# Optimization experiments

Hardware: AMD Instinct MI355X
Metric: run time of the kernel (lower is better)

Reference implementation:

```python
import jax, jax.numpy as jnp
import numpy as np

B, SQ, SK, D, H = 4, 2048, 2048, 1024, 16
HD = D // H
SCALE = HD ** -0.5


def setup_inputs() -> dict:
    key = jax.random.key(0)
    ks = jax.random.split(key, 11)
    s = 0.02
    return {
        "query": jax.random.normal(ks[0], (B, SQ, D), jnp.float32),
        "key": jax.random.normal(ks[1], (B, SK, D), jnp.float32),
        "value": jax.random.normal(ks[2], (B, SK, D), jnp.float32),
        "Wq": jax.random.normal(ks[3], (D, D), jnp.float32) * s,
        "bq": jnp.zeros((D,), jnp.float32),
        "Wk": jax.random.normal(ks[4], (D, D), jnp.float32) * s,
        "bk": jnp.zeros((D,), jnp.float32),
        "Wv": jax.random.normal(ks[5], (D, D), jnp.float32) * s,
        "bv": jnp.zeros((D,), jnp.float32),
        "Wo": jax.random.normal(ks[6], (D, D), jnp.float32) * s,
        "bo": jnp.zeros((D,), jnp.float32),
    }


def reference(query, key, value, Wq, bq, Wk, bk, Wv, bv, Wo, bo):
    # Linear projections (torch nn.Linear: x @ W.T + b)
    Q = query @ Wq.T + bq          # (B, SQ, D)
    K = key @ Wk.T + bk            # (B, SK, D)
    V = value @ Wv.T + bv          # (B, SK, D)
    # split heads -> (B, H, S, HD)
    Q = Q.reshape(B, SQ, H, HD).transpose(0, 2, 1, 3)
    K = K.reshape(B, SK, H, HD).transpose(0, 2, 1, 3)
    V = V.reshape(B, SK, H, HD).transpose(0, 2, 1, 3)
    scores = jnp.einsum('bhqd,bhkd->bhqk', Q, K) * SCALE
    attn = jax.nn.softmax(scores, axis=-1)     # (B, H, SQ, SK); dropout=0 (eval)
    attended = jnp.einsum('bhqk,bhkd->bhqd', attn, V)
    attended = attended.mean(axis=1)           # head-average -> (B, SQ, HD)
    attended = jnp.tile(attended, (1, 1, H))   # repeat to (B, SQ, D)
    output = attended @ Wo.T + bo
    avg_attention = attn.mean(axis=1)          # (B, SQ, SK)
    return (output, avg_attention)
```

## Files before the change

### kernel.cpp

```cpp
#include <hip/hip_runtime.h>
#include <hip/hip_bf16.h>
#include <math.h>

#define BB 4
#define SQL 2048
#define SKL 2048
#define DM 1024
#define NH 16
#define HDIM 64
#define QSCALE 0.18033688011112042f

typedef __attribute__((ext_vector_type(8))) short bf16x8;
typedef __attribute__((ext_vector_type(4))) float f32x4;
typedef __attribute__((ext_vector_type(16))) float f32x16;

__device__ __forceinline__ float exp2fast(float x) { return __builtin_amdgcn_exp2f(x); }
__device__ __forceinline__ float log2fast(float x) { return __builtin_amdgcn_logf(x); }

__device__ __forceinline__ unsigned short f2bf(float f) {
    union { __hip_bfloat16 h; unsigned short u; } c;
    c.h = __float2bfloat16(f);
    return c.u;
}

__device__ __forceinline__ unsigned cvtpk(float lo, float hi) {
    unsigned r;
    asm("v_cvt_pk_bf16_f32 %0, %1, %2" : "=v"(r) : "v"(lo), "v"(hi));
    return r;
}

__device__ __forceinline__ bf16x8 cvt8(const float4& a, const float4& b) {
    bf16x8 r;
    r[0] = (short)f2bf(a.x); r[1] = (short)f2bf(a.y);
    r[2] = (short)f2bf(a.z); r[3] = (short)f2bf(a.w);
    r[4] = (short)f2bf(b.x); r[5] = (short)f2bf(b.y);
    r[6] = (short)f2bf(b.z); r[7] = (short)f2bf(b.w);
    return r;
}

__device__ __forceinline__ void gload16(const void* g, void* l) {
    __builtin_amdgcn_global_load_lds(
        (const __attribute__((address_space(1))) unsigned int*)g,
        (__attribute__((address_space(3))) unsigned int*)l, 16, 0, 0);
}

#define VMCNT0() asm volatile("s_waitcnt vmcnt(0)" ::: "memory")

__global__ __launch_bounds__(256)
void wo_eff_kernel(const float* __restrict__ Wo, float* __restrict__ We) {
    int i = blockIdx.x * 256 + threadIdx.x;
    if (i < DM * HDIM) {
        int n = i >> 6, d = i & 63;
        float s = 0.f;
#pragma unroll
        for (int h = 0; h < NH; ++h) s += Wo[(size_t)n * DM + h * HDIM + d];
        We[i] = s;
    }
}

__global__ __launch_bounds__(256)
void proj_bf16(const float* __restrict__ X, const float* __restrict__ W,
               const float* __restrict__ bias, unsigned short* __restrict__ Y,
               float scale)
{
    __shared__ __align__(16) unsigned short As[128 * 32];
    __shared__ __align__(16) unsigned short Bs[128 * 32];
    const int tid = threadIdx.x;
    const int lane = tid & 63, wid = tid >> 6;
    const int g = lane >> 4, lm = lane & 15;
    const int wr = wid >> 1, wc = wid & 1;
    const int m0 = blockIdx.x * 128, n0 = blockIdx.y * 128;

    int rA[2], cA[2], offA[2];
#pragma unroll
    for (int i = 0; i < 2; ++i) {
        int q = tid + i * 256;
        rA[i] = q >> 2; cA[i] = q & 3;
        offA[i] = rA[i] * 32 + ((cA[i] ^ (rA[i] & 3)) << 3);
    }
    float4 xa[2][2], wa[2][2], xb[2][2], wb[2][2];
#pragma unroll
    for (int i = 0; i < 2; ++i) {
        const float* xp = &X[(size_t)(m0 + rA[i]) * DM + cA[i] * 8];
        const float* wp = &W[(size_t)(n0 + rA[i]) * DM + cA[i] * 8];
        xa[i][0] = *(const float4*)xp; xa[i][1] = *(const float4*)(xp + 4);
        wa[i][0] = *(const float4*)wp; wa[i][1] = *(const float4*)(wp + 4);
    }
    const f32x4 fz = {0.f, 0.f, 0.f, 0.f};
    f32x4 acc[4][4];
#pragma unroll
    for (int i = 0; i < 4; ++i)
#pragma unroll
        for (int j = 0; j < 4; ++j) acc[i][j] = fz;

    for (int t = 0; t < 32; ++t) {
        __syncthreads();
#pragma unroll
        for (int i = 0; i < 2; ++i) {
            *(bf16x8*)&As[offA[i]] = cvt8(xa[i][0], xa[i][1]);
            *(bf16x8*)&Bs[offA[i]] = cvt8(wa[i][0], wa[i][1]);
        }
        if (t < 31) {
            int k0 = (t + 1) * 32;
#pragma unroll
            for (int i = 0; i < 2; ++i) {
                const float* xp = &X[(size_t)(m0 + rA[i]) * DM + k0 + cA[i] * 8];
                const float* wp = &W[(size_t)(n0 + rA[i]) * DM + k0 + cA[i] * 8];
                xb[i][0] = *(const float4*)xp; xb[i][1] = *(const float4*)(xp + 4);
                wb[i][0] = *(const float4*)wp; wb[i][1] = *(const float4*)(wp + 4);
            }
        }
        __syncthreads();
        bf16x8 a[4], b[4];
#pragma unroll
        for (int f = 0; f < 4; ++f) {
            int ra = wr * 64 + f * 16 + lm;
            a[f] = *(const bf16x8*)&As[ra * 32 + (((g) ^ (ra & 3)) << 3)];
            int rb = wc * 64 + f * 16 + lm;
            b[f] = *(const bf16x8*)&Bs[rb * 32 + (((g) ^ (rb & 3)) << 3)];
        }
#pragma unroll
        for (int fm = 0; fm < 4; ++fm)
#pragma unroll
            for (int fn = 0; fn < 4; ++fn)
                acc[fm][fn] = __builtin_amdgcn_mfma_f32_16x16x32_bf16(
                    a[fm], b[fn], acc[fm][fn], 0, 0, 0);
        if (t < 31) {
#pragma unroll
            for (int i = 0; i < 2; ++i) {
                xa[i][0] = xb[i][0]; xa[i][1] = xb[i][1];
                wa[i][0] = wb[i][0]; wa[i][1] = wb[i][1];
            }
        }
    }
    float bn[4];
#pragma unroll
    for (int fn = 0; fn < 4; ++fn) bn[fn] = bias[n0 + wc * 64 + fn * 16 + lm];
#pragma unroll
    for (int fm = 0; fm < 4; ++fm)
#pragma unroll
        for (int i = 0; i < 4; ++i) {
            int m = m0 + wr * 64 + fm * 16 + 4 * g + i;
#pragma unroll
            for (int fn = 0; fn < 4; ++fn) {
                int n = n0 + wc * 64 + fn * 16 + lm;
                Y[(size_t)m * DM + n] = f2bf((acc[fm][fn][i] + bn[fn]) * scale);
            }
        }
}

__global__ __launch_bounds__(256)
void transpose_v(const unsigned short* __restrict__ V, unsigned short* __restrict__ Vt)
{
    __shared__ __align__(16) unsigned short Ts[64][80];
    const int tid = threadIdx.x;
    const int kv0 = blockIdx.x * 64, h = blockIdx.y, b = blockIdx.z;
#pragma unroll
    for (int i = 0; i < 2; ++i) {
        int q = tid + i * 256;
        int r = q >> 3, c = q & 7;
        *(uint4*)&Ts[r][c * 8] =
            *(const uint4*)&V[(size_t)(b * SKL + kv0 + r) * DM + h * HDIM + c * 8];
    }
    __syncthreads();
#pragma unroll
    for (int i = 0; i < 2; ++i) {
        int q = tid + i * 256;
        int d = q >> 3, kc = q & 7;
        union { unsigned short u16[8]; uint4 v; } tw;
#pragma unroll
        for (int e = 0; e < 8; ++e) tw.u16[e] = Ts[kc * 8 + e][d];
        *(uint4*)&Vt[((size_t)(b * NH + h) * HDIM + d) * SKL + kv0 + kc * 8] = tw.v;
    }
}

__global__ __launch_bounds__(256, 2)
void flash_mfma2(const unsigned short* __restrict__ Q,
                 const unsigned short* __restrict__ K,
                 const unsigned short* __restrict__ Vt,
                 float* __restrict__ uw, float* __restrict__ O)
{
    __shared__ __align__(16) unsigned short sK[2][64 * 64];
    __shared__ __align__(16) unsigned short sV[2][64 * 64];
    const int tid = threadIdx.x;
    const int lane = tid & 63, wid = tid >> 6;
    const int l31 = lane & 31, h8 = lane >> 5;
    const int L = blockIdx.x + (blockIdx.y << 3) + (blockIdx.z << 7);
    const int f = ((L & 7) << 6) + (L >> 3);
    const int q0 = (f & 7) * 256;
    const int h = (f >> 3) & 15;
    const int b = f >> 7;
    const int myq0 = q0 + wid * 32 + l31;
    const int myq1 = myq0 + 128;

    bf16x8 qf0[4], qf1[4];
    {
        const unsigned short* qp0 = &Q[(size_t)(b * SQL + myq0) * DM + h * HDIM + h8 * 8];
        const unsigned short* qp1 = &Q[(size_t)(b * SQL + myq1) * DM + h * HDIM + h8 * 8];
#pragma unroll
        for (int c = 0; c < 4; ++c) {
            qf0[c] = *(const bf16x8*)(qp0 + c * 16);
            qf1[c] = *(const bf16x8*)(qp1 + c * 16);
        }
    }

    int rr[2], cc[2];
#pragma unroll
    for (int i = 0; i < 2; ++i) {
        int s = tid + i * 256;
        rr[i] = s >> 3;
        cc[i] = ((s & 7) ^ (rr[i] & 7)) * 8;
    }
    const unsigned short* Kbase = &K[((size_t)b * SKL) * DM + h * HDIM];
    const unsigned short* Vbase = &Vt[((size_t)(b * NH + h) * HDIM) * SKL];

#pragma unroll
    for (int i = 0; i < 2; ++i) {
        gload16(Kbase + (size_t)rr[i] * DM + cc[i], &sK[0][(wid * 64 + i * 256) * 8]);
        gload16(Vbase + (size_t)rr[i] * SKL + cc[i], &sV[0][(wid * 64 + i * 256) * 8]);
    }
    VMCNT0();
    __syncthreads();

    const f32x16 z16 = {0.f};
    f32x16 o00 = z16, o01 = z16, o10 = z16, o11 = z16;
    float l0 = 0.f, l1 = 0.f;
    int cur = 0;

    for (int kt = 0; kt < SKL / 64; ++kt) {
        if (kt + 1 < SKL / 64) {
            int k0 = (kt + 1) * 64;
#pragma unroll
            for (int i = 0; i < 2; ++i) {
                gload16(Kbase + (size_t)(k0 + rr[i]) * DM + cc[i],
                        &sK[cur ^ 1][(wid * 64 + i * 256) * 8]);
                gload16(Vbase + (size_t)rr[i] * SKL + k0 + cc[i],
                        &sV[cur ^ 1][(wid * 64 + i * 256) * 8]);
            }
        }
        f32x16 c00 = z16, c01 = z16, c10 = z16, c11 = z16;
        __builtin_amdgcn_s_setprio(1);
#pragma unroll
        for (int c = 0; c < 4; ++c) {
            int cg = 2 * c + h8;
            bf16x8 a0 = *(const bf16x8*)&sK[cur][l31 * 64 + ((cg ^ (l31 & 7)) << 3)];
            bf16x8 a1 = *(const bf16x8*)&sK[cur][(32 + l31) * 64 + ((cg ^ (l31 & 7)) << 3)];
            c00 = __builtin_amdgcn_mfma_f32_32x32x16_bf16(a0, qf0[c], c00, 0, 0, 0);
            c01 = __builtin_amdgcn_mfma_f32_32x32x16_bf16(a1, qf0[c], c01, 0, 0, 0);
            c10 = __builtin_amdgcn_mfma_f32_32x32x16_bf16(a0, qf1[c], c10, 0, 0, 0);
            c11 = __builtin_amdgcn_mfma_f32_32x32x16_bf16(a1, qf1[c], c11, 0, 0, 0);
        }
        __builtin_amdgcn_s_setprio(0);
        bf16x8 ap0[4], ap1[4];
        {
            float ps = 0.f;
#pragma unroll
            for (int r = 0; r < 16; ++r) { c00[r] = exp2fast(c00[r]); ps += c00[r]; }
#pragma unroll
            for (int r = 0; r < 16; ++r) { c01[r] = exp2fast(c01[r]); ps += c01[r]; }
            l0 += ps;
#pragma unroll
            for (int ks = 0; ks < 4; ++ks) {
                const int base = (ks & 1) * 8;
                const f32x16& ct = (ks & 2) ? c01 : c00;
                unsigned wA0 = cvtpk(ct[base + 0], ct[base + 1]);
                unsigned wA1 = cvtpk(ct[base + 2], ct[base + 3]);
                unsigned wB0 = cvtpk(ct[base + 4], ct[base + 5]);
                unsigned wB1 = cvtpk(ct[base + 6], ct[base + 7]);
                asm volatile("v_permlane32_swap_b32 %0, %1" : "+v"(wA0), "+v"(wB0));
                asm volatile("v_permlane32_swap_b32 %0, %1" : "+v"(wA1), "+v"(wB1));
                union { unsigned u[4]; bf16x8 v; } pu;
                pu.u[0] = wA0; pu.u[1] = wA1; pu.u[2] = wB0; pu.u[3] = wB1;
                ap0[ks] = pu.v;
            }
        }
        {
            float ps = 0.f;
#pragma unroll
            for (int r = 0; r < 16; ++r) { c10[r] = exp2fast(c10[r]); ps += c10[r]; }
#pragma unroll
            for (int r = 0; r < 16; ++r) { c11[r] = exp2fast(c11[r]); ps += c11[r]; }
            l1 += ps;
#pragma unroll
            for (int ks = 0; ks < 4; ++ks) {
                const int base = (ks & 1) * 8;
                const f32x16& ct = (ks & 2) ? c11 : c10;
                unsigned wA0 = cvtpk(ct[base + 0], ct[base + 1]);
                unsigned wA1 = cvtpk(ct[base + 2], ct[base + 3]);
                unsigned wB0 = cvtpk(ct[base + 4], ct[base + 5]);
                unsigned wB1 = cvtpk(ct[base + 6], ct[base + 7]);
                asm volatile("v_permlane32_swap_b32 %0, %1" : "+v"(wA0), "+v"(wB0));
                asm volatile("v_permlane32_swap_b32 %0, %1" : "+v"(wA1), "+v"(wB1));
                union { unsigned u[4]; bf16x8 v; } pu;
                pu.u[0] = wA0; pu.u[1] = wA1; pu.u[2] = wB0; pu.u[3] = wB1;
                ap1[ks] = pu.v;
            }
        }
        __builtin_amdgcn_s_setprio(1);
#pragma unroll
        for (int ks = 0; ks < 4; ++ks) {
            int cg = 2 * ks + h8;
            bf16x8 v0 = *(const bf16x8*)&sV[cur][l31 * 64 + ((cg ^ (l31 & 7)) << 3)];
            bf16x8 v1 = *(const bf16x8*)&sV[cur][(32 + l31) * 64 + ((cg ^ (l31 & 7)) << 3)];
            o00 = __builtin_amdgcn_mfma_f32_32x32x16_bf16(v0, ap0[ks], o00, 0, 0, 0);
            o01 = __builtin_amdgcn_mfma_f32_32x32x16_bf16(v1, ap0[ks], o01, 0, 0, 0);
            o10 = __builtin_amdgcn_mfma_f32_32x32x16_bf16(v0, ap1[ks], o10, 0, 0, 0);
            o11 = __builtin_amdgcn_mfma_f32_32x32x16_bf16(v1, ap1[ks], o11, 0, 0, 0);
        }
        __builtin_amdgcn_s_setprio(0);
        VMCNT0();
        __syncthreads();
        cur ^= 1;
    }

    l0 += __shfl_xor(l0, 32);
    l1 += __shfl_xor(l1, 32);
    if (h8 == 0) {
        uw[(size_t)(b * NH + h) * SQL + myq0] = log2fast(l0 * (float)NH);
        uw[(size_t)(b * NH + h) * SQL + myq1] = log2fast(l1 * (float)NH);
    }
    const float inv0 = 1.0f / (l0 * (float)NH);
    const float inv1 = 1.0f / (l1 * (float)NH);
    float* Op0 = &O[((size_t)(b * NH + h) * SQL + myq0) * HDIM];
    float* Op1 = &O[((size_t)(b * NH + h) * SQL + myq1) * HDIM];
#pragma unroll
    for (int i2 = 0; i2 < 4; ++i2) {
        float4 w0, w1;
        int d = 8 * i2 + 4 * h8;
        w0.x = o00[4 * i2 + 0] * inv0; w0.y = o00[4 * i2 + 1] * inv0;
        w0.z = o00[4 * i2 + 2] * inv0; w0.w = o00[4 * i2 + 3] * inv0;
        w1.x = o01[4 * i2 + 0] * inv0; w1.y = o01[4 * i2 + 1] * inv0;
        w1.z = o01[4 * i2 + 2] * inv0; w1.w = o01[4 * i2 + 3] * inv0;
        *(float4*)(Op0 + d) = w0;
        *(float4*)(Op0 + d + 32) = w1;
        w0.x = o10[4 * i2 + 0] * inv1; w0.y = o10[4 * i2 + 1] * inv1;
        w0.z = o10[4 * i2 + 2] * inv1; w0.w = o10[4 * i2 + 3] * inv1;
        w1.x = o11[4 * i2 + 0] * inv1; w1.y = o11[4 * i2 + 1] * inv1;
        w1.z = o11[4 * i2 + 2] * inv1; w1.w = o11[4 * i2 + 3] * inv1;
        *(float4*)(Op1 + d) = w0;
        *(float4*)(Op1 + d + 32) = w1;
    }
}

__global__ __launch_bounds__(256)
void am_reduce(const float* __restrict__ O, float* __restrict__ am)
{
    int i = blockIdx.x * 256 + threadIdx.x;
    int bq = i >> 4, c = i & 15;
    int b = bq >> 11, q = bq & 2047;
    const float* base = O + ((size_t)b * NH * SQL + q) * HDIM + c * 4;
    float4 s = {0.f, 0.f, 0.f, 0.f};
    for (int h = 0; h < NH; ++h) {
        float4 v = *(const float4*)(base + (size_t)h * SQL * HDIM);
        s.x += v.x; s.y += v.y; s.z += v.z; s.w += v.w;
    }
    *(float4*)(am + (size_t)bq * HDIM + c * 4) = s;
}

__global__ __launch_bounds__(512)
void avg_mfma2(const unsigned short* __restrict__ Q, const unsigned short* __restrict__ K,
               const float* __restrict__ uw, float* __restrict__ avg)
{
    __shared__ __align__(16) unsigned short sQ[2][128 * 64];
    __shared__ __align__(16) unsigned short sK[2][128 * 64];
    __shared__ float uS[NH][128];
    const int tid = threadIdx.x;
    const int lane = tid & 63, wid = tid >> 6;
    const int g = lane >> 4, lm = lane & 15;
    const int wq = wid >> 1, wk = wid & 1;
    const int L = blockIdx.x + (blockIdx.y << 4) + (blockIdx.z << 8);
    const int f = ((L & 7) << 7) + (L >> 3);
    const int k0 = (f & 15) * 128;
    const int q0 = ((f >> 4) & 15) * 128;
    const int b = f >> 8;

    for (int i = tid; i < NH * 128; i += 512) {
        int hh = i >> 7, qq = i & 127;
        uS[hh][qq] = uw[(size_t)(b * NH + hh) * SQL + q0 + qq];
    }

    int rs[2], cs[2];
#pragma unroll
    for (int i = 0; i < 2; ++i) {
        int s = tid + i * 512;
        rs[i] = s >> 3;
        cs[i] = (s & 7) ^ (rs[i] & 7);
    }
    const unsigned short* Qbase = &Q[(size_t)(b * SQL + q0) * DM];
    const unsigned short* Kbase = &K[(size_t)(b * SKL + k0) * DM];
#pragma unroll
    for (int i = 0; i < 2; ++i) {
        gload16(Qbase + (size_t)rs[i] * DM + cs[i] * 8, &sQ[0][(tid + i * 512) * 8]);
        gload16(Kbase + (size_t)rs[i] * DM + cs[i] * 8, &sK[0][(tid + i * 512) * 8]);
    }
    VMCNT0();
    __syncthreads();

    const f32x4 fz = {0.f, 0.f, 0.f, 0.f};
    f32x4 acc[2][4];
#pragma unroll
    for (int mf = 0; mf < 2; ++mf)
#pragma unroll
        for (int nf = 0; nf < 4; ++nf) acc[mf][nf] = fz;

    int cur = 0;
    for (int hh = 0; hh < NH; ++hh) {
        if (hh + 1 < NH) {
#pragma unroll
            for (int i = 0; i < 2; ++i) {
                gload16(Qbase + (size_t)rs[i] * DM + (hh + 1) * HDIM + cs[i] * 8,
                        &sQ[cur ^ 1][(tid + i * 512) * 8]);
                gload16(Kbase + (size_t)rs[i] * DM + (hh + 1) * HDIM + cs[i] * 8,
                        &sK[cur ^ 1][(tid + i * 512) * 8]);
            }
        }
        f32x4 s[2][4];
#pragma unroll
        for (int mf = 0; mf < 2; ++mf)
#pragma unroll
            for (int nf = 0; nf < 4; ++nf) s[mf][nf] = fz;
        __builtin_amdgcn_s_setprio(1);
#pragma unroll
        for (int kk = 0; kk < 2; ++kk) {
            bf16x8 a[2];
#pragma unroll
            for (int mf = 0; mf < 2; ++mf) {
                int ra = wq * 32 + mf * 16 + lm;
                a[mf] = *(const bf16x8*)&sQ[cur][ra * 64 + (((kk * 4 + g) ^ (ra & 7)) << 3)];
            }
#pragma unroll
            for (int nf = 0; nf < 4; ++nf) {
                int rb = wk * 64 + nf * 16 + lm;
                bf16x8 kb = *(const bf16x8*)&sK[cur][rb * 64 + (((kk * 4 + g) ^ (rb & 7)) << 3)];
#pragma unroll
                for (int mf = 0; mf < 2; ++mf)
                    s[mf][nf] = __builtin_amdgcn_mfma_f32_16x16x32_bf16(
                        a[mf], kb, s[mf][nf], 0, 0, 0);
            }
        }
        __builtin_amdgcn_s_setprio(0);
#pragma unroll
        for (int mf = 0; mf < 2; ++mf)
#pragma unroll
            for (int i4 = 0; i4 < 4; ++i4) {
                float u = uS[hh][wq * 32 + mf * 16 + 4 * g + i4];
#pragma unroll
                for (int nf = 0; nf < 4; ++nf)
                    acc[mf][nf][i4] += exp2fast(s[mf][nf][i4] - u);
            }
        VMCNT0();
        __syncthreads();
        cur ^= 1;
    }
#pragma unroll
    for (int mf = 0; mf < 2; ++mf)
#pragma unroll
        for (int i4 = 0; i4 < 4; ++i4) {
            int qrow = q0 + wq * 32 + mf * 16 + 4 * g + i4;
#pragma unroll
            for (int nf = 0; nf < 4; ++nf)
                avg[(size_t)(b * SQL + qrow) * SKL + k0 + wk * 64 + nf * 16 + lm] =
                    acc[mf][nf][i4];
        }
}

__global__ __launch_bounds__(256)
void out_gemm(const float* __restrict__ amp, const float* __restrict__ We,
              const float* __restrict__ bo, float* __restrict__ out)
{
    __shared__ float As[64][68];
    __shared__ float Bs[64][68];
    const int m0 = blockIdx.x << 6, n0 = blockIdx.y << 6;
    const int tid = threadIdx.x;
    const int tx = tid & 15, ty = tid >> 4;
    const int lrow = tid >> 4, ldc = (tid & 15) << 2;
#pragma unroll
    for (int rr = 0; rr < 4; ++rr) {
        int r = (rr << 4) + lrow;
        float4 a = *reinterpret_cast<const float4*>(&amp[(size_t)(m0 + r) * HDIM + ldc]);
        float4 w = *reinterpret_cast<const float4*>(&We[(size_t)(n0 + r) * HDIM + ldc]);
        As[ldc + 0][r] = a.x; As[ldc + 1][r] = a.y; As[ldc + 2][r] = a.z; As[ldc + 3][r] = a.w;
        Bs[ldc + 0][r] = w.x; Bs[ldc + 1][r] = w.y; Bs[ldc + 2][r] = w.z; Bs[ldc + 3][r] = w.w;
    }
    __syncthreads();
    float acc[4][4] = {};
    for (int d = 0; d < 64; ++d) {
        float4 av = *reinterpret_cast<const float4*>(&As[d][ty << 2]);
        float4 bv = *reinterpret_cast<const float4*>(&Bs[d][tx << 2]);
        float aa[4] = {av.x, av.y, av.z, av.w};
        float bb[4] = {bv.x, bv.y, bv.z, bv.w};
#pragma unroll
        for (int i = 0; i < 4; ++i)
#pragma unroll
            for (int j = 0; j < 4; ++j)
                acc[i][j] = fmaf(aa[i], bb[j], acc[i][j]);
    }
    float4 bv = *reinterpret_cast<const float4*>(&bo[n0 + (tx << 2)]);
    float bb4[4] = {bv.x, bv.y, bv.z, bv.w};
#pragma unroll
    for (int i = 0; i < 4; ++i) {
        int m = m0 + (ty << 2) + i;
        float4 o = make_float4(acc[i][0] + bb4[0], acc[i][1] + bb4[1],
                               acc[i][2] + bb4[2], acc[i][3] + bb4[3]);
        *reinterpret_cast<float4*>(&out[(size_t)m * DM + n0 + (tx << 2)]) = o;
    }
}

extern "C" void kernel_launch(void* const* d_in, const int* in_sizes, int n_in,
                              void* d_out, int out_size, void* d_ws, size_t ws_size,
                              hipStream_t stream)
{
    const float* query = (const float*)d_in[0];
    const float* key   = (const float*)d_in[1];
    const float* value = (const float*)d_in[2];
    const float* Wq = (const float*)d_in[3];
    const float* bq = (const float*)d_in[4];
    const float* Wk = (const float*)d_in[5];
    const float* bk = (const float*)d_in[6];
    const float* Wv = (const float*)d_in[7];
    const float* bv = (const float*)d_in[8];
    const float* Wo = (const float*)d_in[9];
    const float* bo = (const float*)d_in[10];

    float* out0 = (float*)d_out;
    float* out_avg = out0 + (size_t)BB * SQL * DM;

    const size_t nQ = (size_t)BB * SQL * DM;
    const size_t nML = (size_t)BB * NH * SQL;
    const size_t nAM = (size_t)BB * SQL * HDIM;
    unsigned short* Qb = (unsigned short*)d_ws;
    unsigned short* Kb = Qb + nQ;
    unsigned short* Vb = Kb + nQ;
    unsigned short* Vt = Vb + nQ;
    float* Ob  = (float*)(Vt + nQ);
    float* uw  = Ob + (size_t)BB * NH * SQL * HDIM;
    float* amb = uw + nML;
    float* We  = amb + nAM;

    dim3 blk(256);
    wo_eff_kernel<<<dim3((DM * HDIM + 255) / 256), blk, 0, stream>>>(Wo, We);

    dim3 gp(64, 8);
    proj_bf16<<<gp, blk, 0, stream>>>(query, Wq, bq, Qb, QSCALE);
    proj_bf16<<<gp, blk, 0, stream>>>(key,   Wk, bk, Kb, 1.0f);
    proj_bf16<<<gp, blk, 0, stream>>>(value, Wv, bv, Vb, 1.0f);

    transpose_v<<<dim3(32, 16, 4), blk, 0, stream>>>(Vb, Vt);
    flash_mfma2<<<dim3(SQL / 256, NH, BB), blk, 0, stream>>>(Qb, Kb, Vt, uw, Ob);
    am_reduce<<<dim3(512), blk, 0, stream>>>(Ob, amb);
    avg_mfma2<<<dim3(SKL / 128, SQL / 128, BB), dim3(512), 0, stream>>>(Qb, Kb, uw, out_avg);
    out_gemm<<<dim3(128, 16), blk, 0, stream>>>(amb, We, bo, out0);
}
```

Baseline: 297.0 us.

## Use 128-key tiles in flash kernel and interleave PV with softmax; relayout O

```diff
diff --git a/kernel.cpp b/kernel.cpp
--- a/kernel.cpp
+++ b/kernel.cpp
@@ -180,8 +180,8 @@
                  const unsigned short* __restrict__ Vt,
                  float* __restrict__ uw, float* __restrict__ O)
 {
-    __shared__ __align__(16) unsigned short sK[2][64 * 64];
-    __shared__ __align__(16) unsigned short sV[2][64 * 64];
+    __shared__ __align__(16) unsigned short sK[2][128 * 64];
+    __shared__ __align__(16) unsigned short sV[2][64 * 128];
     const int tid = threadIdx.x;
     const int lane = tid & 63, wid = tid >> 6;
     const int l31 = lane & 31, h8 = lane >> 5;
@@ -204,20 +204,22 @@
         }
     }
 
-    int rr[2], cc[2];
-#pragma unroll
-    for (int i = 0; i < 2; ++i) {
+    int krr[4], kcc[4], vrr[4], vcc[4];
+#pragma unroll
+    for (int i = 0; i < 4; ++i) {
         int s = tid + i * 256;
-        rr[i] = s >> 3;
-        cc[i] = ((s & 7) ^ (rr[i] & 7)) * 8;
+        krr[i] = s >> 3;
+        kcc[i] = ((s & 7) ^ (krr[i] & 7)) * 8;
+        vrr[i] = s >> 4;
+        vcc[i] = ((s & 15) ^ (vrr[i] & 15)) * 8;
     }
     const unsigned short* Kbase = &K[((size_t)b * SKL) * DM + h * HDIM];
     const unsigned short* Vbase = &Vt[((size_t)(b * NH + h) * HDIM) * SKL];
 
 #pragma unroll
-    for (int i = 0; i < 2; ++i) {
-        gload16(Kbase + (size_t)rr[i] * DM + cc[i], &sK[0][(wid * 64 + i * 256) * 8]);
-        gload16(Vbase + (size_t)rr[i] * SKL + cc[i], &sV[0][(wid * 64 + i * 256) * 8]);
+    for (int i = 0; i < 4; ++i) {
+        gload16(Kbase + (size_t)krr[i] * DM + kcc[i], &sK[0][(wid * 64 + i * 256) * 8]);
+        gload16(Vbase + (size_t)vrr[i] * SKL + vcc[i], &sV[0][(wid * 64 + i * 256) * 8]);
     }
     VMCNT0();
     __syncthreads();
@@ -227,87 +229,99 @@
     float l0 = 0.f, l1 = 0.f;
     int cur = 0;
 
-    for (int kt = 0; kt < SKL / 64; ++kt) {
-        if (kt + 1 < SKL / 64) {
-            int k0 = (kt + 1) * 64;
-#pragma unroll
-            for (int i = 0; i < 2; ++i) {
-                gload16(Kbase + (size_t)(k0 + rr[i]) * DM + cc[i],
+    for (int kt = 0; kt < SKL / 128; ++kt) {
+        if (kt + 1 < SKL / 128) {
+            int kk0 = (kt + 1) * 128;
+#pragma unroll
+            for (int i = 0; i < 4; ++i) {
+                gload16(Kbase + (size_t)(kk0 + krr[i]) * DM + kcc[i],
                         &sK[cur ^ 1][(wid * 64 + i * 256) * 8]);
-                gload16(Vbase + (size_t)rr[i] * SKL + k0 + cc[i],
+                gload16(Vbase + (size_t)vrr[i] * SKL + kk0 + vcc[i],
                         &sV[cur ^ 1][(wid * 64 + i * 256) * 8]);
             }
         }
-        f32x16 c00 = z16, c01 = z16, c10 = z16, c11 = z16;
-        __builtin_amdgcn_s_setprio(1);
-#pragma unroll
-        for (int c = 0; c < 4; ++c) {
-            int cg = 2 * c + h8;
-            bf16x8 a0 = *(const bf16x8*)&sK[cur][l31 * 64 + ((cg ^ (l31 & 7)) << 3)];
-            bf16x8 a1 = *(const bf16x8*)&sK[cur][(32 + l31) * 64 + ((cg ^ (l31 & 7)) << 3)];
-            c00 = __builtin_amdgcn_mfma_f32_32x32x16_bf16(a0, qf0[c], c00, 0, 0, 0);
-            c01 = __builtin_amdgcn_mfma_f32_32x32x16_bf16(a1, qf0[c], c01, 0, 0, 0);
-            c10 = __builtin_amdgcn_mfma_f32_32x32x16_bf16(a0, qf1[c], c10, 0, 0, 0);
-            c11 = __builtin_amdgcn_mfma_f32_32x32x16_bf16(a1, qf1[c], c11, 0, 0, 0);
-        }
-        __builtin_amdgcn_s_setprio(0);
-        bf16x8 ap0[4], ap1[4];
         {
+            f32x16 c[4] = {z16, z16, z16, z16};
+            __builtin_amdgcn_s_setprio(1);
+#pragma unroll
+            for (int dc = 0; dc < 4; ++dc) {
+                int cg = 2 * dc + h8;
+#pragma unroll
+                for (int j = 0; j < 4; ++j) {
+                    int r = 32 * j + l31;
+                    bf16x8 a = *(const bf16x8*)&sK[cur][r * 64 + ((cg ^ (r & 7)) << 3)];
+                    c[j] = __builtin_amdgcn_mfma_f32_32x32x16_bf16(a, qf0[dc], c[j], 0, 0, 0);
+                }
+            }
+            __builtin_amdgcn_s_setprio(0);
             float ps = 0.f;
 #pragma unroll
-            for (int r = 0; r < 16; ++r) { c00[r] = exp2fast(c00[r]); ps += c00[r]; }
-#pragma unroll
-            for (int r = 0; r < 16; ++r) { c01[r] = exp2fast(c01[r]); ps += c01[r]; }
+            for (int j = 0; j < 4; ++j)
+#pragma unroll
+                for (int r = 0; r < 16; ++r) { c[j][r] = exp2fast(c[j][r]); ps += c[j][r]; }
             l0 += ps;
-#pragma unroll
-            for (int ks = 0; ks < 4; ++ks) {
-                const int base = (ks & 1) * 8;
-                const f32x16& ct = (ks & 2) ? c01 : c00;
-                unsigned wA0 = cvtpk(ct[base + 0], ct[base + 1]);
-                unsigned wA1 = cvtpk(ct[base + 2], ct[base + 3]);
-                unsigned wB0 = cvtpk(ct[base + 4], ct[base + 5]);
-                unsigned wB1 = cvtpk(ct[base + 6], ct[base + 7]);
+            __builtin_amdgcn_s_setprio(1);
+#pragma unroll
+            for (int ks = 0; ks < 8; ++ks) {
+                const int j = ks >> 1, base = (ks & 1) * 8;
+                unsigned wA0 = cvtpk(c[j][base + 0], c[j][base + 1]);
+                unsigned wA1 = cvtpk(c[j][base + 2], c[j][base + 3]);
+                unsigned wB0 = cvtpk(c[j][base + 4], c[j][base + 5]);
+                unsigned wB1 = cvtpk(c[j][base + 6], c[j][base + 7]);
                 asm volatile("v_permlane32_swap_b32 %0, %1" : "+v"(wA0), "+v"(wB0));
                 asm volatile("v_permlane32_swap_b32 %0, %1" : "+v"(wA1), "+v"(wB1));
                 union { unsigned u[4]; bf16x8 v; } pu;
                 pu.u[0] = wA0; pu.u[1] = wA1; pu.u[2] = wB0; pu.u[3] = wB1;
-                ap0[ks] = pu.v;
-            }
+                int ch = 2 * ks + h8;
+                int r0 = l31, r1 = 32 + l31;
+                bf16x8 v0 = *(const bf16x8*)&sV[cur][r0 * 128 + ((ch ^ (r0 & 15)) << 3)];
+                bf16x8 v1 = *(const bf16x8*)&sV[cur][r1 * 128 + ((ch ^ (r1 & 15)) << 3)];
+                o00 = __builtin_amdgcn_mfma_f32_32x32x16_bf16(v0, pu.v, o00, 0, 0, 0);
+                o01 = __builtin_amdgcn_mfma_f32_32x32x16_bf16(v1, pu.v, o01, 0, 0, 0);
+            }
+            __builtin_amdgcn_s_setprio(0);
         }
         {
+            f32x16 c[4] = {z16, z16, z16, z16};
+            __builtin_amdgcn_s_setprio(1);
+#pragma unroll
+            for (int dc = 0; dc < 4; ++dc) {
+                int cg = 2 * dc + h8;
+#pragma unroll
+                for (int j = 0; j < 4; ++j) {
+                    int r = 32 * j + l31;
+                    bf16x8 a = *(const bf16x8*)&sK[cur][r * 64 + ((cg ^ (r & 7)) << 3)];
+                    c[j] = __builtin_amdgcn_mfma_f32_32x32x16_bf16(a, qf1[dc], c[j], 0, 0, 0);
+                }
+            }
+            __builtin_amdgcn_s_setprio(0);
             float ps = 0.f;
 #pragma unroll
-            for (int r = 0; r < 16; ++r) { c10[r] = exp2fast(c10[r]); ps += c10[r]; }
-#pragma unroll
-            for (int r = 0; r < 16; ++r) { c11[r] = exp2fast(c11[r]); ps += c11[r]; }
+            for (int j = 0; j < 4; ++j)
+#pragma unroll
+                for (int r = 0; r < 16; ++r) { c[j][r] = exp2fast(c[j][r]); ps += c[j][r]; }
             l1 += ps;
-#pragma unroll
-            for (int ks = 0; ks < 4; ++ks) {
-                const int base = (ks & 1) * 8;
-                const f32x16& ct = (ks & 2) ? c11 : c10;
-                unsigned wA0 = cvtpk(ct[base + 0], ct[base + 1]);
-                unsigned wA1 = cvtpk(ct[base + 2], ct[base + 3]);
-                unsigned wB0 = cvtpk(ct[base + 4], ct[base + 5]);
-                unsigned wB1 = cvtpk(ct[base + 6], ct[base + 7]);
+            __builtin_amdgcn_s_setprio(1);
+#pragma unroll
+            for (int ks = 0; ks < 8; ++ks) {
+                const int j = ks >> 1, base = (ks & 1) * 8;
+                unsigned wA0 = cvtpk(c[j][base + 0], c[j][base + 1]);
+                unsigned wA1 = cvtpk(c[j][base + 2], c[j][base + 3]);
+                unsigned wB0 = cvtpk(c[j][base + 4], c[j][base + 5]);
+                unsigned wB1 = cvtpk(c[j][base + 6], c[j][base + 7]);
                 asm volatile("v_permlane32_swap_b32 %0, %1" : "+v"(wA0), "+v"(wB0));
                 asm volatile("v_permlane32_swap_b32 %0, %1" : "+v"(wA1), "+v"(wB1));
                 union { unsigned u[4]; bf16x8 v; } pu;
                 pu.u[0] = wA0; pu.u[1] = wA1; pu.u[2] = wB0; pu.u[3] = wB1;
-                ap1[ks] = pu.v;
-            }
-        }
-        __builtin_amdgcn_s_setprio(1);
-#pragma unroll
-        for (int ks = 0; ks < 4; ++ks) {
-            int cg = 2 * ks + h8;
-            bf16x8 v0 = *(const bf16x8*)&sV[cur][l31 * 64 + ((cg ^ (l31 & 7)) << 3)];
-            bf16x8 v1 = *(const bf16x8*)&sV[cur][(32 + l31) * 64 + ((cg ^ (l31 & 7)) << 3)];
-            o00 = __builtin_amdgcn_mfma_f32_32x32x16_bf16(v0, ap0[ks], o00, 0, 0, 0);
-            o01 = __builtin_amdgcn_mfma_f32_32x32x16_bf16(v1, ap0[ks], o01, 0, 0, 0);
-            o10 = __builtin_amdgcn_mfma_f32_32x32x16_bf16(v0, ap1[ks], o10, 0, 0, 0);
-            o11 = __builtin_amdgcn_mfma_f32_32x32x16_bf16(v1, ap1[ks], o11, 0, 0, 0);
-        }
-        __builtin_amdgcn_s_setprio(0);
+                int ch = 2 * ks + h8;
+                int r0 = l31, r1 = 32 + l31;
+                bf16x8 v0 = *(const bf16x8*)&sV[cur][r0 * 128 + ((ch ^ (r0 & 15)) << 3)];
+                bf16x8 v1 = *(const bf16x8*)&sV[cur][r1 * 128 + ((ch ^ (r1 & 15)) << 3)];
+                o10 = __builtin_amdgcn_mfma_f32_32x32x16_bf16(v0, pu.v, o10, 0, 0, 0);
+                o11 = __builtin_amdgcn_mfma_f32_32x32x16_bf16(v1, pu.v, o11, 0, 0, 0);
+            }
+            __builtin_amdgcn_s_setprio(0);
+        }
         VMCNT0();
         __syncthreads();
         cur ^= 1;
@@ -321,8 +335,8 @@
     }
     const float inv0 = 1.0f / (l0 * (float)NH);
     const float inv1 = 1.0f / (l1 * (float)NH);
-    float* Op0 = &O[((size_t)(b * NH + h) * SQL + myq0) * HDIM];
-    float* Op1 = &O[((size_t)(b * NH + h) * SQL + myq1) * HDIM];
+    float* Op0 = &O[((size_t)(b * SQL + myq0) * NH + h) * HDIM];
+    float* Op1 = &O[((size_t)(b * SQL + myq1) * NH + h) * HDIM];
 #pragma unroll
     for (int i2 = 0; i2 < 4; ++i2) {
         float4 w0, w1;
@@ -347,11 +361,11 @@
 {
     int i = blockIdx.x * 256 + threadIdx.x;
     int bq = i >> 4, c = i & 15;
-    int b = bq >> 11, q = bq & 2047;
-    const float* base = O + ((size_t)b * NH * SQL + q) * HDIM + c * 4;
+    const float* base = O + (size_t)bq * NH * HDIM + c * 4;
     float4 s = {0.f, 0.f, 0.f, 0.f};
+#pragma unroll
     for (int h = 0; h < NH; ++h) {
-        float4 v = *(const float4*)(base + (size_t)h * SQL * HDIM);
+        float4 v = *(const float4*)(base + h * HDIM);
         s.x += v.x; s.y += v.y; s.z += v.z; s.w += v.w;
     }
     *(float4*)(am + (size_t)bq * HDIM + c * 4) = s;
```

After: 334.6 us. 1.13x slower.
